# Optimization experiments

Hardware: AMD Instinct MI355X
Metric: run time of the kernel (lower is better)

## Reference

```python
import jax, jax.numpy as jnp
import numpy as np

N = 500_000      # total nodes (vehicles + obstacles)
NV = 400_000     # vehicles, stored as prefix rows [:NV]
E = 16_000_000   # directed edges

DT = 0.2
SAFE = 1.5
PARK = 5.0
RADIUS = 1.5
DEFV = 2.5
BOUND0 = 1.0
BOUND1 = 0.8
PI = np.pi


def setup_inputs() -> dict:
    key = jax.random.key(0)
    k1, k2, k3, k4, k5 = jax.random.split(key, 5)
    y_pred = jax.random.normal(k1, (NV, 2), jnp.float32)
    y_ref = jax.random.normal(k2, (NV, 2), jnp.float32)
    X = jax.random.normal(k3, (N, 9), jnp.float32)
    # type flag in last column: 0 = vehicle (prefix), 1 = obstacle
    type_col = jnp.concatenate([jnp.zeros(NV, jnp.float32), jnp.ones(N - NV, jnp.float32)])
    X_cur = X.at[:, 8].set(type_col)
    edges = jax.random.randint(k4, (2, E), 0, N, dtype=jnp.int32)
    be_static = jax.random.normal(k5, (NV, 2), jnp.float32)
    return {"y_pred": y_pred, "y_ref": y_ref, "X_cur": X_cur, "edges": edges, "be_static": be_static}


def _vehicle_dynamic(X, y, nv):
    # X: [N, 9], y: [nv, 2] controls (pedal, steer); vehicles are rows [:nv]
    cur = X[:nv]
    x_t = cur[:, 0] + cur[:, 3] * jnp.cos(cur[:, 2]) * DT
    y_t = cur[:, 1] + cur[:, 3] * jnp.sin(cur[:, 2]) * DT
    psi_t = cur[:, 2] + cur[:, 3] * DT * jnp.tan(y[:, 1]) / 2.0
    psi_t = (psi_t + PI) % (2 * PI) - PI
    v_t = 0.99 * cur[:, 3] + y[:, 0] * DT
    nxt = jnp.stack([x_t, y_t, psi_t, v_t], axis=-1)
    veh = jnp.concatenate([nxt, cur[:, 4:]], axis=1)
    return jnp.concatenate([veh, X[nv:]], axis=0)


def _loss_for_speed(X_ref, theta_ref, pedal_ref, pedal_pred, edges, nv, n):
    e0, e1 = edges[0], edges[1]
    veh_e = (e0 < nv).astype(X_ref.dtype)          # [E] edge-source-is-vehicle
    speed = X_ref[:, 3].at[:nv].add((pedal_pred - pedal_ref) * DT)  # [N]
    safe = jnp.abs(speed[e1]) + veh_e * jnp.abs(speed[e0]) + SAFE   # [E]
    vec = jnp.stack([jnp.cos(theta_ref), jnp.sin(theta_ref)], axis=-1)  # [nv,2]
    pos_pred_v = X_ref[:nv, :2] + vec * speed[:nv, None] * DT
    pos_pred = jnp.concatenate([pos_pred_v, X_ref[nv:, :2]], axis=0)    # [N,2]
    col7 = X_ref[:, 7]

    def col_loss(pos):
        d = jnp.linalg.norm(pos[e0] - pos[e1], axis=-1)
        lc = jax.nn.relu(safe + col7[e0] + (veh_e + 1.0) * RADIUS - d)
        lc = lc * lc + lc
        return jax.ops.segment_sum(lc, e1, num_segments=n)[:nv]

    loss_pred = jnp.linalg.norm(pos_pred_v, axis=-1) + col_loss(pos_pred)
    loss_ref = jnp.linalg.norm(X_ref[:nv, :2], axis=-1) + col_loss(X_ref[:, :2])
    d = loss_pred - loss_ref
    m = (d >= 0).astype(d.dtype)
    return (d * d + d) * m + d * (1.0 - m)


def reference(y_pred, y_ref, X_cur, edges, be_static):
    nv = y_pred.shape[0]
    n = X_cur.shape[0]
    X_ref = _vehicle_dynamic(X_cur, y_ref, nv)
    mask_1 = (jnp.linalg.norm(X_ref[:nv, :2] - X_cur[:nv, 4:6], axis=-1)
              - (PARK + jnp.abs(X_cur[:nv, 3]))) > 0
    mask_2 = jnp.abs(X_ref[:nv, 3]) >= DEFV - 1e-05
    mask_3 = jnp.sign(X_ref[:nv, 3]) * (y_ref[:, 0] - y_pred[:, 0]) <= 1e-05
    mask = (mask_1 & mask_2 & mask_3).astype(y_pred.dtype)

    loss_1 = jnp.mean(((y_ref[:, 1] - y_pred[:, 1]) / BOUND1) ** 2)
    loss_2_1 = ((y_ref[:, 0] - y_pred[:, 0]) / BOUND0) ** 2
    loss_2_2 = _loss_for_speed(X_ref, y_ref[:, 1], y_ref[:, 0], y_pred[:, 0], edges, nv, n)
    loss_2 = jnp.mean(loss_2_1 * (1.0 - mask) + loss_2_2 * mask)
    loss = loss_1 + loss_2

    bound = jnp.array([BOUND0, BOUND1], dtype=be_static.dtype)
    loss_3 = jnp.sum((be_static / bound) ** 2, axis=-1)
    loss = loss + jnp.mean(loss_3) * 0.1
    return loss
```

## Files before the change

kernel.cpp:

```cpp
#include <hip/hip_runtime.h>
#include <math.h>

#define NVEH 400000
#define NTOT 500000
#define NEDGE 16000000
#define DT 0.2f
#define SAFE_C 1.5f
#define PARK_C 5.0f
#define RADIUS_C 1.5f
#define DEFV_C 2.5f
#define LIST_CAP 4096
#define LIST_USE 128
#define REG_USE 16

#define NODE_BLOCKS ((NTOT + 255) / 256)
#define NODE_WAVES  (NODE_BLOCKS * 4)


__global__ __launch_bounds__(256) void node_kernel(
    const float* __restrict__ yp, const float* __restrict__ yr,
    const float* __restrict__ X, const float* __restrict__ be,
    float4* __restrict__ pos, float2* __restrict__ gh,
    float* __restrict__ basediff, float* __restrict__ maskArr,
    int* __restrict__ countp, int* __restrict__ ids,
    double* __restrict__ partials)
{
    int i = blockIdx.x * blockDim.x + threadIdx.x;
    double local = 0.0;
    if (i < NTOT) {
        const float* row = X + (size_t)i * 9;
        if (i < NVEH) {
            float x0 = row[0], x1 = row[1], psi = row[2], v = row[3];
            float p4 = row[4], p5 = row[5], x7 = row[7];
            float yr0 = yr[2 * i], yr1 = yr[2 * i + 1];
            float yp0 = yp[2 * i], yp1 = yp[2 * i + 1];

            float xt = x0 + v * cosf(psi) * DT;
            float yt = x1 + v * sinf(psi) * DT;
            float vt = 0.99f * v + yr0 * DT;

            float speed = vt + (yp0 - yr0) * DT;
            float ct = cosf(yr1), st = sinf(yr1);
            float ppx = xt + ct * speed * DT;
            float ppy = yt + st * speed * DT;

            float as = fabsf(speed);
            pos[i] = make_float4(ppx, ppy, xt, yt);
            gh[i]  = make_float2(x7 + RADIUS_C + as + RADIUS_C, as + SAFE_C);

            float nrm_pred = sqrtf(ppx * ppx + ppy * ppy);
            float nrm_ref  = sqrtf(xt * xt + yt * yt);
            basediff[i] = nrm_pred - nrm_ref;

            float dx = xt - p4, dy = yt - p5;
            bool m1 = (sqrtf(dx * dx + dy * dy) - (PARK_C + fabsf(v))) > 0.0f;
            bool m2 = fabsf(vt) >= (DEFV_C - 1e-5f);
            float sg = (vt > 0.0f) ? 1.0f : ((vt < 0.0f) ? -1.0f : 0.0f);
            bool m3 = sg * (yr0 - yp0) <= 1e-5f;
            bool msk = m1 && m2 && m3;
            maskArr[i] = msk ? 1.0f : 0.0f;
            if (msk) {
                int idx = atomicAdd(countp, 1);
                if (idx < LIST_CAP) ids[idx] = i;
            }

            float t1 = (yr1 - yp1) * 1.25f;
            float l1 = t1 * t1;
            float t2 = yr0 - yp0;
            float l21 = t2 * t2;
            float b0 = be[2 * i], b1 = be[2 * i + 1];
            float b1s = b1 * 1.25f;
            float l3 = b0 * b0 + b1s * b1s;

            local = (double)l1 + (double)((msk ? 0.0f : 1.0f) * l21) + 0.1 * (double)l3;
        } else {
            float x0 = row[0], x1 = row[1], v = row[3], x7 = row[7];
            pos[i] = make_float4(x0, x1, x0, x1);
            gh[i]  = make_float2(x7 + RADIUS_C, fabsf(v) + SAFE_C);
        }
    }
    for (int off = 32; off > 0; off >>= 1)
        local += __shfl_down(local, off, 64);
    if ((threadIdx.x & 63) == 0)
        partials[blockIdx.x * 4 + (threadIdx.x >> 6)] = local;
}

__device__ __forceinline__ void edge_compute(
    int a, int b, const float4* __restrict__ pos, const float2* __restrict__ gh,
    float* __restrict__ segdiff)
{
    float4 pa = pos[a];
    float4 pb = pos[b];
    float base = gh[a].x + gh[b].y;

    float dxp = pa.x - pb.x, dyp = pa.y - pb.y;
    float dp = sqrtf(dxp * dxp + dyp * dyp);
    float lcp = fmaxf(base - dp, 0.0f);

    float dxr = pa.z - pb.z, dyr = pa.w - pb.w;
    float dr = sqrtf(dxr * dxr + dyr * dyr);
    float lcr = fmaxf(base - dr, 0.0f);

    float diff = (lcp * lcp + lcp) - (lcr * lcr + lcr);
    if (diff != 0.0f)
        atomicAdd(segdiff + b, diff);
}

__global__ __launch_bounds__(256) void edge_kernel(
    const int* __restrict__ e0p, const int* __restrict__ e1p,
    const float4* __restrict__ pos, const float2* __restrict__ gh,
    const float* __restrict__ maskArr,
    float* __restrict__ segdiff,
    const int* __restrict__ countp, const int* __restrict__ ids)
{
    __shared__ int s_ids[LIST_USE];
    int cnt = *countp;
    int base = (blockIdx.x * 256 + threadIdx.x) * 4;

    if (cnt <= LIST_USE) {
        if (threadIdx.x < cnt) s_ids[threadIdx.x] = ids[threadIdx.x];
        __syncthreads();
        int4 bv = *(const int4*)(e1p + base);

        if (cnt <= REG_USE) {
            int idr[REG_USE];
#pragma unroll
            for (int j = 0; j < REG_USE; ++j)
                idr[j] = (j < cnt) ? s_ids[j] : -1;

            int bs[4] = {bv.x, bv.y, bv.z, bv.w};
#pragma unroll
            for (int k = 0; k < 4; ++k) {
                int b = bs[k];
                bool h = false;
#pragma unroll
                for (int j = 0; j < REG_USE; ++j) h |= (b == idr[j]);
                if (h) {
                    int a = e0p[base + k];
                    edge_compute(a, b, pos, gh, segdiff);
                }
            }
        } else {
            int bs[4] = {bv.x, bv.y, bv.z, bv.w};
#pragma unroll
            for (int k = 0; k < 4; ++k) {
                int b = bs[k];
                bool h = false;
                for (int j = 0; j < cnt; ++j) h |= (b == s_ids[j]);
                if (h) {
                    int a = e0p[base + k];
                    edge_compute(a, b, pos, gh, segdiff);
                }
            }
        }
    } else {
        for (int k = 0; k < 4; ++k) {
            int b = e1p[base + k];
            if (b < NVEH && maskArr[b] != 0.0f) {
                int a = e0p[base + k];
                edge_compute(a, b, pos, gh, segdiff);
            }
        }
    }
}

__global__ __launch_bounds__(256) void finish_kernel(
    const double* __restrict__ partials,
    const float* __restrict__ basediff, const float* __restrict__ segdiff,
    const float* __restrict__ maskArr,
    const int* __restrict__ countp, const int* __restrict__ ids,
    float* __restrict__ out)
{
    int tid = threadIdx.x;
    double s = 0.0;
    for (int j = tid; j < NODE_WAVES; j += 256)
        s += partials[j];

    int cnt = *countp;
    if (cnt <= LIST_CAP) {
        for (int j = tid; j < cnt; j += 256) {
            int i = ids[j];
            float d = basediff[i] + segdiff[i];
            s += (double)((d >= 0.0f) ? (d * d + d) : d);
        }
    } else {
        for (int i = tid; i < NVEH; i += 256) {
            if (maskArr[i] != 0.0f) {
                float d = basediff[i] + segdiff[i];
                s += (double)((d >= 0.0f) ? (d * d + d) : d);
            }
        }
    }

    __shared__ double red[4];
    for (int off = 32; off > 0; off >>= 1)
        s += __shfl_down(s, off, 64);
    if ((tid & 63) == 0) red[tid >> 6] = s;
    __syncthreads();
    if (tid == 0) {
        double t = red[0] + red[1] + red[2] + red[3];
        out[0] = (float)(t * (1.0 / (double)NVEH));
    }
}

extern "C" void kernel_launch(void* const* d_in, const int* in_sizes, int n_in,
                              void* d_out, int out_size, void* d_ws, size_t ws_size,
                              hipStream_t stream) {
    const float* yp = (const float*)d_in[0];
    const float* yr = (const float*)d_in[1];
    const float* X  = (const float*)d_in[2];
    const int*   ed = (const int*)d_in[3];
    const float* be = (const float*)d_in[4];
    float* out = (float*)d_out;

    char* ws = (char*)d_ws;
    float4* pos      = (float4*)(ws + 0);
    float2* gh       = (float2*)(ws + 8000000);
    float*  basediff = (float*) (ws + 12000000);
    float*  maskArr  = (float*) (ws + 13600000);
    float*  segdiff  = (float*) (ws + 15200000);
    int*    countp   = (int*)   (ws + 16800000);
    int*    ids      = (int*)   (ws + 16800016);
    double* partials = (double*)(ws + 16816400);

    hipMemsetAsync(segdiff, 0, 1600004, stream);

    node_kernel<<<NODE_BLOCKS, 256, 0, stream>>>(
        yp, yr, X, be, pos, gh, basediff, maskArr, countp, ids, partials);

    edge_kernel<<<NEDGE / (256 * 4), 256, 0, stream>>>(
        ed, ed + NEDGE, pos, gh, maskArr, segdiff, countp, ids);

    finish_kernel<<<1, 256, 0, stream>>>(
        partials, basediff, segdiff, maskArr, countp, ids, out);
}
```

Baseline: 208.2 us.

## Stage X rows through shared memory, zero segdiff only for masked nodes

The node kernel now loads each block's 9-float rows into shared memory with coalesced float4 reads, and reads the yr, yp and be pairs as float2. The 1.6 MB memset of segdiff is replaced by a 4-byte memset of the counter, with segdiff zeroed only at masked vehicle indices, the only ones read later. The finish kernel unrolls its partials reduction into four accumulators. The fallback path still relies on maskArr filtering, so unmasked entries are never read; the float4 staging assumes each block's row offset in X is 16-byte aligned.

```diff
diff --git a/kernel.cpp b/kernel.cpp
--- a/kernel.cpp
+++ b/kernel.cpp
@@ -22,18 +22,31 @@
     const float* __restrict__ X, const float* __restrict__ be,
     float4* __restrict__ pos, float2* __restrict__ gh,
     float* __restrict__ basediff, float* __restrict__ maskArr,
+    float* __restrict__ segdiff,
     int* __restrict__ countp, int* __restrict__ ids,
     double* __restrict__ partials)
 {
-    int i = blockIdx.x * blockDim.x + threadIdx.x;
+    __shared__ float sX[256 * 9];
+    int blk0 = blockIdx.x * 256;
+    int nrows = NTOT - blk0; if (nrows > 256) nrows = 256;
+    {
+        int nf4 = (nrows * 9) >> 2;
+        const float4* src = (const float4*)(X + (size_t)blk0 * 9);
+        for (int t = threadIdx.x; t < nf4; t += 256)
+            ((float4*)sX)[t] = src[t];
+    }
+    __syncthreads();
+
+    int i = blk0 + threadIdx.x;
     double local = 0.0;
     if (i < NTOT) {
-        const float* row = X + (size_t)i * 9;
+        const float* row = sX + threadIdx.x * 9;
         if (i < NVEH) {
             float x0 = row[0], x1 = row[1], psi = row[2], v = row[3];
             float p4 = row[4], p5 = row[5], x7 = row[7];
-            float yr0 = yr[2 * i], yr1 = yr[2 * i + 1];
-            float yp0 = yp[2 * i], yp1 = yp[2 * i + 1];
+            float2 yrv = ((const float2*)yr)[i];
+            float2 ypv = ((const float2*)yp)[i];
+            float yr0 = yrv.x, yr1 = yrv.y, yp0 = ypv.x, yp1 = ypv.y;
 
             float xt = x0 + v * cosf(psi) * DT;
             float yt = x1 + v * sinf(psi) * DT;
@@ -60,6 +73,7 @@
             bool msk = m1 && m2 && m3;
             maskArr[i] = msk ? 1.0f : 0.0f;
             if (msk) {
+                segdiff[i] = 0.0f;
                 int idx = atomicAdd(countp, 1);
                 if (idx < LIST_CAP) ids[idx] = i;
             }
@@ -68,9 +82,9 @@
             float l1 = t1 * t1;
             float t2 = yr0 - yp0;
             float l21 = t2 * t2;
-            float b0 = be[2 * i], b1 = be[2 * i + 1];
-            float b1s = b1 * 1.25f;
-            float l3 = b0 * b0 + b1s * b1s;
+            float2 bev = ((const float2*)be)[i];
+            float b1s = bev.y * 1.25f;
+            float l3 = bev.x * bev.x + b1s * b1s;
 
             local = (double)l1 + (double)((msk ? 0.0f : 1.0f) * l21) + 0.1 * (double)l3;
         } else {
@@ -172,9 +186,14 @@
     float* __restrict__ out)
 {
     int tid = threadIdx.x;
-    double s = 0.0;
-    for (int j = tid; j < NODE_WAVES; j += 256)
-        s += partials[j];
+    double s0 = 0.0, s1 = 0.0, s2 = 0.0, s3 = 0.0;
+    for (int j = tid; j < NODE_WAVES; j += 1024) {
+        s0 += partials[j];
+        if (j + 256 < NODE_WAVES) s1 += partials[j + 256];
+        if (j + 512 < NODE_WAVES) s2 += partials[j + 512];
+        if (j + 768 < NODE_WAVES) s3 += partials[j + 768];
+    }
+    double s = (s0 + s1) + (s2 + s3);
 
     int cnt = *countp;
     if (cnt <= LIST_CAP) {
@@ -223,10 +242,10 @@
     int*    ids      = (int*)   (ws + 16800016);
     double* partials = (double*)(ws + 16816400);
 
-    hipMemsetAsync(segdiff, 0, 1600004, stream);
+    hipMemsetAsync(countp, 0, 4, stream);
 
     node_kernel<<<NODE_BLOCKS, 256, 0, stream>>>(
-        yp, yr, X, be, pos, gh, basediff, maskArr, countp, ids, partials);
+        yp, yr, X, be, pos, gh, basediff, maskArr, segdiff, countp, ids, partials);
 
     edge_kernel<<<NEDGE / (256 * 4), 256, 0, stream>>>(
         ed, ed + NEDGE, pos, gh, maskArr, segdiff, countp, ids);
```

New measurement: 203.2 us. -2.4%, faster.
